# Performance work log

Measured on AMD Instinct MI355X. Metric: run time of the kernel, lower is better.

The kernel has to match this reference:

```python
import jax, jax.numpy as jnp
import numpy as np

B, L, D, H = 2, 2048, 1024, 16
DH = D // H  # 64


def setup_inputs() -> dict:
    key = jax.random.key(0)
    ks = jax.random.split(key, 11)
    s = 0.02
    return {
        "src": jax.random.normal(ks[0], (B, L, D), dtype=jnp.float32),
        "Wq": jax.random.normal(ks[1], (D, D), dtype=jnp.float32) * s,
        "bq": jax.random.normal(ks[2], (D,), dtype=jnp.float32) * s,
        "Wk": jax.random.normal(ks[3], (D, D), dtype=jnp.float32) * s,
        "bk": jax.random.normal(ks[4], (D,), dtype=jnp.float32) * s,
        "Wv": jax.random.normal(ks[5], (D, D), dtype=jnp.float32) * s,
        "bv": jax.random.normal(ks[6], (D,), dtype=jnp.float32) * s,
        "Wo": jax.random.normal(ks[7], (D, D), dtype=jnp.float32) * s,
        "bo": jax.random.normal(ks[8], (D,), dtype=jnp.float32) * s,
        "conv_w": jax.random.normal(ks[9], (H, D, 3), dtype=jnp.float32) * s,  # Conv1d weight [out=H, in=D, k=3]
        "conv_b": jax.random.normal(ks[10], (H,), dtype=jnp.float32) * s,
    }


def reference(src, Wq, bq, Wk, bk, Wv, bv, Wo, bo, conv_w, conv_b):
    b, l, d = src.shape
    h, dh = H, DH
    # QKV projections (torch Linear: x @ W.T + b), split into heads: [B,H,L,DH]
    Q = (src @ Wq.T + bq).reshape(b, l, h, dh).transpose(0, 2, 1, 3)
    K = (src @ Wk.T + bk).reshape(b, l, h, dh).transpose(0, 2, 1, 3)
    V = (src @ Wv.T + bv).reshape(b, l, h, dh).transpose(0, 2, 1, 3)
    # saliency conv: Conv1d(D->H, k=3, padding='same') on [B,D,L] -> [B,H,L]
    sal = jax.lax.conv_general_dilated(
        src.transpose(0, 2, 1), conv_w,
        window_strides=(1,), padding=[(1, 1)],
        dimension_numbers=("NCH", "OIH", "NCH"),
    ) + conv_b[None, :, None]
    # attention scores + per-head saliency bias (broadcast over query axis)
    scores = jnp.einsum("bhqd,bhkd->bhqk", Q, K) / jnp.sqrt(jnp.float32(dh))
    scores = scores + sal[:, :, None, :]
    attn = jax.nn.softmax(scores, axis=-1)  # dropout is identity in eval
    out = jnp.einsum("bhqk,bhkd->bhqd", attn, V)  # [B,H,L,DH]
    out = out.transpose(0, 2, 1, 3).reshape(b, l, d)
    out = out @ Wo.T + bo
    return out, attn
```

## Files before the change

kernel.cpp:

```cpp
#include <hip/hip_runtime.h>

typedef __bf16 bf16x8 __attribute__((ext_vector_type(8)));
typedef float f32x4 __attribute__((ext_vector_type(4)));
typedef unsigned short u16;
typedef unsigned int u32;

#define MFMA(a, b, c) __builtin_amdgcn_mfma_f32_16x16x32_bf16((a), (b), (c), 0, 0, 0)


__device__ __forceinline__ u16 f2bf(float f) {
  u32 u = __float_as_uint(f);
  return (u16)((u + 0x7fffu + ((u >> 16) & 1u)) >> 16);
}

__global__ __launch_bounds__(256) void prep_all(
    const float4* __restrict__ src, const float4* __restrict__ wq,
    const float4* __restrict__ wk, const float4* __restrict__ wv,
    const float4* __restrict__ wo, const float* __restrict__ cw,
    uint2* __restrict__ srcb, uint2* __restrict__ wqb, uint2* __restrict__ wkb,
    uint2* __restrict__ wvb, uint2* __restrict__ wob, float* __restrict__ cwT) {
  int bx = blockIdx.x;
  if (bx < 8192) {
    const float4* in;
    uint2* out;
    int base;
    if (bx < 4096) { in = src; out = srcb; base = 0; }
    else if (bx < 5120) { in = wq; out = wqb; base = 4096; }
    else if (bx < 6144) { in = wk; out = wkb; base = 5120; }
    else if (bx < 7168) { in = wv; out = wvb; base = 6144; }
    else { in = wo; out = wob; base = 7168; }
    int i = (bx - base) * 256 + threadIdx.x;
    float4 v = in[i];
    uint2 o;
    o.x = (u32)f2bf(v.x) | ((u32)f2bf(v.y) << 16);
    o.y = (u32)f2bf(v.z) | ((u32)f2bf(v.w) << 16);
    out[i] = o;
  } else {
    int i = (bx - 8192) * 256 + threadIdx.x;
    int h = i / 3072;
    int j = (i - h * 3072) >> 10;
    int d = i & 1023;
    cwT[i] = cw[(h * 1024 + d) * 3 + j];
  }
}

__global__ __launch_bounds__(256) void conv_sal_k(const float* __restrict__ src,
                                                  const float* __restrict__ cwT,
                                                  const float* __restrict__ cb,
                                                  float* __restrict__ sal) {
  const int t = threadIdx.x;
  const int h = t & 15, li = t >> 4;
  const int b = blockIdx.y;
  const int l = blockIdx.x * 16 + li;
  float4 acc = {0.f, 0.f, 0.f, 0.f};
#pragma unroll
  for (int j = 0; j < 3; j++) {
    int ls = l + j - 1;
    if (ls < 0 || ls >= 2048) continue;
    const float4* sp = (const float4*)(src + ((size_t)b * 2048 + ls) * 1024);
    const float4* wp = (const float4*)(cwT + (h * 3 + j) * 1024);
    for (int d = 0; d < 256; d++) {
      float4 a = sp[d], w = wp[d];
      acc.x += a.x * w.x;
      acc.y += a.y * w.y;
      acc.z += a.z * w.z;
      acc.w += a.w * w.w;
    }
  }
  sal[(b * 16 + h) * 2048 + l] = cb[h] + ((acc.x + acc.y) + (acc.z + acc.w));
}

__device__ __forceinline__ void gemm_core(const u16* __restrict__ Xg, const u16* __restrict__ Wg,
                                          int mblk, int nblk, u16* smA, u16* smB,
                                          f32x4 acc[4][4]) {
  const int t = threadIdx.x;
  const int lane = t & 63, wid = t >> 6;
  const int cl = lane & 15, gp = lane >> 4;
  const int r0 = t >> 2, cc = (t & 3) * 8;
  const u16* gA0 = Xg + (size_t)(mblk + r0) * 1024 + cc;
  const u16* gB0 = Wg + (size_t)(nblk + r0) * 1024 + cc;
  u16* lA0 = smA + t * 8;
  u16* lB0 = smB + t * 8;
  const u16* rA = smA + ((wid >> 1) * 64 + cl) * 32 + gp * 8;
  const u16* rB = smB + ((wid & 1) * 64 + cl) * 32 + gp * 8;
  for (int k0 = 0; k0 < 1024; k0 += 32) {
    bf16x8 sa0 = *(const bf16x8*)(gA0 + k0);
    bf16x8 sa1 = *(const bf16x8*)(gA0 + 64 * 1024 + k0);
    bf16x8 sb0 = *(const bf16x8*)(gB0 + k0);
    bf16x8 sb1 = *(const bf16x8*)(gB0 + 64 * 1024 + k0);
    __syncthreads();
    *(bf16x8*)lA0 = sa0;
    *(bf16x8*)(lA0 + 2048) = sa1;
    *(bf16x8*)lB0 = sb0;
    *(bf16x8*)(lB0 + 2048) = sb1;
    __syncthreads();
    bf16x8 a[4], b[4];
#pragma unroll
    for (int i = 0; i < 4; i++) {
      a[i] = *(const bf16x8*)(rA + i * 512);
      b[i] = *(const bf16x8*)(rB + i * 512);
    }
#pragma unroll
    for (int tm = 0; tm < 4; tm++)
#pragma unroll
      for (int tn = 0; tn < 4; tn++) acc[tm][tn] = MFMA(a[tm], b[tn], acc[tm][tn]);
  }
}

__global__ __launch_bounds__(256) void qkv_gemm(
    const u16* __restrict__ Xb, const u16* __restrict__ Wqb, const u16* __restrict__ Wkb,
    const u16* __restrict__ Wvb, const float* __restrict__ bq, const float* __restrict__ bk,
    const float* __restrict__ bv, u16* __restrict__ Qb, u16* __restrict__ Kb,
    u16* __restrict__ Vt) {
  __shared__ __align__(16) u16 smA[4096], smB[4096];
  const int seg = blockIdx.x >> 3;
  const u16* __restrict__ W = (seg == 0) ? Wqb : (seg == 1) ? Wkb : Wvb;
  const float* __restrict__ bias = (seg == 0) ? bq : (seg == 1) ? bk : bv;
  const int lane = threadIdx.x & 63, wid = threadIdx.x >> 6;
  const int cl = lane & 15, gp = lane >> 4;
  const int mblk = blockIdx.y * 128, nblk = (blockIdx.x & 7) * 128;
  const int m0 = mblk + (wid >> 1) * 64;
  const int n0 = nblk + (wid & 1) * 64;
  f32x4 acc[4][4] = {};
  gemm_core(Xb, W, mblk, nblk, smA, smB, acc);
#pragma unroll
  for (int tn = 0; tn < 4; tn++) {
    int col = n0 + tn * 16 + cl;
    float bv_ = bias[col];
    int hh = col >> 6, dh = col & 63;
#pragma unroll
    for (int tm = 0; tm < 4; tm++) {
#pragma unroll
      for (int r = 0; r < 4; r++) {
        int row = m0 + tm * 16 + gp * 4 + r;
        u16 hv = f2bf(acc[tm][tn][r] + bv_);
        int bb = row >> 11, l = row & 2047;
        if (seg == 0)
          Qb[(((size_t)(bb * 16 + hh) * 2048 + l) << 6) + dh] = hv;
        else if (seg == 1)
          Kb[(((size_t)(bb * 16 + hh) * 2048 + l) << 6) + dh] = hv;
        else
          Vt[((size_t)(bb * 16 + hh) * 64 + dh) * 2048 + l] = hv;
      }
    }
  }
}

__global__ __launch_bounds__(256) void out_gemm(const u16* __restrict__ Xb,
                                                const u16* __restrict__ W,
                                                const float* __restrict__ bias,
                                                float* __restrict__ Y) {
  __shared__ __align__(16) u16 smA[4096], smB[4096];
  const int lane = threadIdx.x & 63, wid = threadIdx.x >> 6;
  const int cl = lane & 15, gp = lane >> 4;
  const int mblk = blockIdx.y * 128, nblk = blockIdx.x * 128;
  const int m0 = mblk + (wid >> 1) * 64;
  const int n0 = nblk + (wid & 1) * 64;
  f32x4 acc[4][4] = {};
  gemm_core(Xb, W, mblk, nblk, smA, smB, acc);
#pragma unroll
  for (int tn = 0; tn < 4; tn++) {
    int col = n0 + tn * 16 + cl;
    float bv_ = bias[col];
#pragma unroll
    for (int tm = 0; tm < 4; tm++)
#pragma unroll
      for (int r = 0; r < 4; r++) {
        int row = m0 + tm * 16 + gp * 4 + r;
        Y[(size_t)row * 1024 + col] = acc[tm][tn][r] + bv_;
      }
  }
}

__global__ __launch_bounds__(256) void flash_fused(const u16* __restrict__ Qb,
                                                   const u16* __restrict__ Kb,
                                                   const u16* __restrict__ Vt,
                                                   const float* __restrict__ sal,
                                                   float* __restrict__ attn,
                                                   u16* __restrict__ Ob) {
  __shared__ __align__(16) u16 pbuf[4][16][72];
  const int bh = blockIdx.x;
  const int b = bh >> 4, h = bh & 15;
  const int lane = threadIdx.x & 63, wid = threadIdx.x >> 6;
  const int cl = lane & 15, gp = lane >> 4;
  const int q0 = blockIdx.y * 64 + wid * 16;
  const u16* Qh = Qb + (size_t)bh * 2048 * 64;
  const u16* Kh = Kb + (size_t)bh * 2048 * 64;
  const u16* Vh = Vt + (size_t)bh * 64 * 2048;
  const float* salh = sal + bh * 2048;
  bf16x8 aQ0 = *(const bf16x8*)(Qh + (size_t)(q0 + cl) * 64 + gp * 8);
  bf16x8 aQ1 = *(const bf16x8*)(Qh + (size_t)(q0 + cl) * 64 + 32 + gp * 8);
  float m[4], l[4];
#pragma unroll
  for (int r = 0; r < 4; r++) { m[r] = -1e30f; l[r] = 0.f; }

  for (int kb = 0; kb < 2048; kb += 64) {
    f32x4 st[4];
#pragma unroll
    for (int tn = 0; tn < 4; tn++) {
      const u16* kp = Kh + (size_t)(kb + tn * 16 + cl) * 64 + gp * 8;
      f32x4 s = {};
      s = MFMA(aQ0, *(const bf16x8*)kp, s);
      s = MFMA(aQ1, *(const bf16x8*)(kp + 32), s);
      st[tn] = s;
    }
#pragma unroll
    for (int tn = 0; tn < 4; tn++) {
      float sv = salh[kb + tn * 16 + cl];
#pragma unroll
      for (int r = 0; r < 4; r++) st[tn][r] = st[tn][r] * 0.125f + sv;
    }
#pragma unroll
    for (int r = 0; r < 4; r++) {
      float v = fmaxf(fmaxf(st[0][r], st[1][r]), fmaxf(st[2][r], st[3][r]));
      v = fmaxf(v, __shfl_xor(v, 1));
      v = fmaxf(v, __shfl_xor(v, 2));
      v = fmaxf(v, __shfl_xor(v, 4));
      v = fmaxf(v, __shfl_xor(v, 8));
      float mn = fmaxf(m[r], v);
      float alpha = __expf(m[r] - mn);
      m[r] = mn;
      float s0 = 0.f;
#pragma unroll
      for (int tn = 0; tn < 4; tn++) s0 += __expf(st[tn][r] - mn);
      s0 += __shfl_xor(s0, 1);
      s0 += __shfl_xor(s0, 2);
      s0 += __shfl_xor(s0, 4);
      s0 += __shfl_xor(s0, 8);
      l[r] = l[r] * alpha + s0;
    }
  }
  float il[4];
#pragma unroll
  for (int r = 0; r < 4; r++) il[r] = 1.0f / l[r];

  f32x4 oacc[4] = {};
  float* arow = attn + (size_t)bh * 2048 * 2048;
  u16* pw = &pbuf[wid][0][0];
  for (int kb = 0; kb < 2048; kb += 64) {
    f32x4 st[4];
#pragma unroll
    for (int tn = 0; tn < 4; tn++) {
      const u16* kp = Kh + (size_t)(kb + tn * 16 + cl) * 64 + gp * 8;
      f32x4 s = {};
      s = MFMA(aQ0, *(const bf16x8*)kp, s);
      s = MFMA(aQ1, *(const bf16x8*)(kp + 32), s);
      st[tn] = s;
    }
#pragma unroll
    for (int tn = 0; tn < 4; tn++) {
      float sv = salh[kb + tn * 16 + cl];
#pragma unroll
      for (int r = 0; r < 4; r++) {
        float p = __expf(st[tn][r] * 0.125f + sv - m[r]);
        arow[(size_t)(q0 + gp * 4 + r) * 2048 + kb + tn * 16 + cl] = p * il[r];
        pw[(gp * 4 + r) * 72 + tn * 16 + cl] = f2bf(p);
      }
    }
    __syncthreads();
    bf16x8 aP0 = *(const bf16x8*)(pw + cl * 72 + gp * 8);
    bf16x8 aP1 = *(const bf16x8*)(pw + cl * 72 + 32 + gp * 8);
#pragma unroll
    for (int tn = 0; tn < 4; tn++) {
      const u16* vp = Vh + (size_t)(tn * 16 + cl) * 2048 + kb + gp * 8;
      oacc[tn] = MFMA(aP0, *(const bf16x8*)vp, oacc[tn]);
      oacc[tn] = MFMA(aP1, *(const bf16x8*)(vp + 32), oacc[tn]);
    }
    __syncthreads();
  }
#pragma unroll
  for (int tn = 0; tn < 4; tn++) {
    int d = h * 64 + tn * 16 + cl;
#pragma unroll
    for (int r = 0; r < 4; r++) {
      int q = q0 + gp * 4 + r;
      Ob[((size_t)(b * 2048 + q)) * 1024 + d] = f2bf(oacc[tn][r] * il[r]);
    }
  }
}

extern "C" void kernel_launch(void* const* d_in, const int* in_sizes, int n_in,
                              void* d_out, int out_size, void* d_ws, size_t ws_size,
                              hipStream_t stream) {
  const float* src = (const float*)d_in[0];
  const float* Wq = (const float*)d_in[1];
  const float* bq = (const float*)d_in[2];
  const float* Wk = (const float*)d_in[3];
  const float* bk = (const float*)d_in[4];
  const float* Wv = (const float*)d_in[5];
  const float* bv = (const float*)d_in[6];
  const float* Wo = (const float*)d_in[7];
  const float* bo = (const float*)d_in[8];
  const float* cw = (const float*)d_in[9];
  const float* cb = (const float*)d_in[10];

  char* ws = (char*)d_ws;
  u16* srcb = (u16*)(ws + 0);
  u16* wqb = (u16*)(ws + 8388608);
  u16* wkb = (u16*)(ws + 10485760);
  u16* wvb = (u16*)(ws + 12582912);
  u16* wob = (u16*)(ws + 14680064);
  u16* Qb = (u16*)(ws + 16777216);
  u16* Kb = (u16*)(ws + 25165824);
  u16* Vt = (u16*)(ws + 33554432);
  u16* Ob = (u16*)(ws + 41943040);
  float* cwT = (float*)(ws + 50331648);
  float* sal = (float*)(ws + 50528256);

  float* outp = (float*)d_out;
  float* attn = (float*)d_out + 4194304;

  prep_all<<<8384, 256, 0, stream>>>((const float4*)src, (const float4*)Wq, (const float4*)Wk,
                                     (const float4*)Wv, (const float4*)Wo, cw,
                                     (uint2*)srcb, (uint2*)wqb, (uint2*)wkb, (uint2*)wvb,
                                     (uint2*)wob, cwT);
  conv_sal_k<<<dim3(128, 2), 256, 0, stream>>>(src, cwT, cb, sal);
  qkv_gemm<<<dim3(24, 32), 256, 0, stream>>>(srcb, wqb, wkb, wvb, bq, bk, bv, Qb, Kb, Vt);
  flash_fused<<<dim3(32, 32), 256, 0, stream>>>(Qb, Kb, Vt, sal, attn, Ob);
  out_gemm<<<dim3(8, 32), 256, 0, stream>>>(Ob, wob, bo, outp);
}
```

Measured before the change: 1.078 ms.

## Split conv reduction across waves, shrink flash blocks, defer row reductions, drop barriers

The saliency conv now splits the D reduction across four waves and combines partial sums through shared memory, which launches four times as many blocks for more parallelism. The flash attention kernel moves to 128-thread blocks over twice as many query tiles, with a launch-bounds occupancy hint. Its first pass keeps per-lane running max and sum and merges them across lanes only once at the end, instead of shuffling every iteration. The block-wide barriers around the P staging buffer are replaced by a wave-local LDS wait, which relies on each wave touching only its own slice of the buffer.

After: 1.100 ms. Within noise of the previous version (+2.0%).

```diff
diff --git a/kernel.cpp b/kernel.cpp
--- a/kernel.cpp
+++ b/kernel.cpp
@@ -48,18 +48,21 @@
                                                   const float* __restrict__ cwT,
                                                   const float* __restrict__ cb,
                                                   float* __restrict__ sal) {
+  __shared__ float part[4][16][17];
   const int t = threadIdx.x;
-  const int h = t & 15, li = t >> 4;
+  const int h = t & 15;
+  const int li = (t >> 4) & 3;
+  const int dc = t >> 6;
   const int b = blockIdx.y;
-  const int l = blockIdx.x * 16 + li;
+  const int l = blockIdx.x * 4 + li;
   float4 acc = {0.f, 0.f, 0.f, 0.f};
 #pragma unroll
   for (int j = 0; j < 3; j++) {
     int ls = l + j - 1;
     if (ls < 0 || ls >= 2048) continue;
-    const float4* sp = (const float4*)(src + ((size_t)b * 2048 + ls) * 1024);
-    const float4* wp = (const float4*)(cwT + (h * 3 + j) * 1024);
-    for (int d = 0; d < 256; d++) {
+    const float4* sp = (const float4*)(src + ((size_t)b * 2048 + ls) * 1024 + dc * 256);
+    const float4* wp = (const float4*)(cwT + (h * 3 + j) * 1024 + dc * 256);
+    for (int d = 0; d < 64; d++) {
       float4 a = sp[d], w = wp[d];
       acc.x += a.x * w.x;
       acc.y += a.y * w.y;
@@ -67,7 +70,12 @@
       acc.w += a.w * w.w;
     }
   }
-  sal[(b * 16 + h) * 2048 + l] = cb[h] + ((acc.x + acc.y) + (acc.z + acc.w));
+  part[dc][li][h] = (acc.x + acc.y) + (acc.z + acc.w);
+  __syncthreads();
+  if (dc == 0) {
+    float s = cb[h] + ((part[0][li][h] + part[1][li][h]) + (part[2][li][h] + part[3][li][h]));
+    sal[(b * 16 + h) * 2048 + l] = s;
+  }
 }
 
 __device__ __forceinline__ void gemm_core(const u16* __restrict__ Xg, const u16* __restrict__ Wg,
@@ -172,28 +180,28 @@
   }
 }
 
-__global__ __launch_bounds__(256) void flash_fused(const u16* __restrict__ Qb,
-                                                   const u16* __restrict__ Kb,
-                                                   const u16* __restrict__ Vt,
-                                                   const float* __restrict__ sal,
-                                                   float* __restrict__ attn,
-                                                   u16* __restrict__ Ob) {
-  __shared__ __align__(16) u16 pbuf[4][16][72];
+__global__ __launch_bounds__(128, 6) void flash_fused(const u16* __restrict__ Qb,
+                                                      const u16* __restrict__ Kb,
+                                                      const u16* __restrict__ Vt,
+                                                      const float* __restrict__ sal,
+                                                      float* __restrict__ attn,
+                                                      u16* __restrict__ Ob) {
+  __shared__ __align__(16) u16 pbuf[2][16][72];
   const int bh = blockIdx.x;
   const int b = bh >> 4, h = bh & 15;
   const int lane = threadIdx.x & 63, wid = threadIdx.x >> 6;
   const int cl = lane & 15, gp = lane >> 4;
-  const int q0 = blockIdx.y * 64 + wid * 16;
+  const int q0 = blockIdx.y * 32 + wid * 16;
   const u16* Qh = Qb + (size_t)bh * 2048 * 64;
   const u16* Kh = Kb + (size_t)bh * 2048 * 64;
   const u16* Vh = Vt + (size_t)bh * 64 * 2048;
   const float* salh = sal + bh * 2048;
   bf16x8 aQ0 = *(const bf16x8*)(Qh + (size_t)(q0 + cl) * 64 + gp * 8);
   bf16x8 aQ1 = *(const bf16x8*)(Qh + (size_t)(q0 + cl) * 64 + 32 + gp * 8);
-  float m[4], l[4];
-#pragma unroll
-  for (int r = 0; r < 4; r++) { m[r] = -1e30f; l[r] = 0.f; }
-
+
+  float ml[4], ll[4];
+#pragma unroll
+  for (int r = 0; r < 4; r++) { ml[r] = -1e30f; ll[r] = 0.f; }
   for (int kb = 0; kb < 2048; kb += 64) {
     f32x4 st[4];
 #pragma unroll
@@ -213,26 +221,30 @@
 #pragma unroll
     for (int r = 0; r < 4; r++) {
       float v = fmaxf(fmaxf(st[0][r], st[1][r]), fmaxf(st[2][r], st[3][r]));
-      v = fmaxf(v, __shfl_xor(v, 1));
-      v = fmaxf(v, __shfl_xor(v, 2));
-      v = fmaxf(v, __shfl_xor(v, 4));
-      v = fmaxf(v, __shfl_xor(v, 8));
-      float mn = fmaxf(m[r], v);
-      float alpha = __expf(m[r] - mn);
-      m[r] = mn;
-      float s0 = 0.f;
-#pragma unroll
-      for (int tn = 0; tn < 4; tn++) s0 += __expf(st[tn][r] - mn);
-      s0 += __shfl_xor(s0, 1);
-      s0 += __shfl_xor(s0, 2);
-      s0 += __shfl_xor(s0, 4);
-      s0 += __shfl_xor(s0, 8);
-      l[r] = l[r] * alpha + s0;
-    }
-  }
-  float il[4];
-#pragma unroll
-  for (int r = 0; r < 4; r++) il[r] = 1.0f / l[r];
+      float mn = fmaxf(ml[r], v);
+      float alpha = __expf(ml[r] - mn);
+      ml[r] = mn;
+      float s0 = __expf(st[0][r] - mn) + __expf(st[1][r] - mn) + __expf(st[2][r] - mn) +
+                 __expf(st[3][r] - mn);
+      ll[r] = ll[r] * alpha + s0;
+    }
+  }
+  float m[4], il[4];
+#pragma unroll
+  for (int r = 0; r < 4; r++) {
+    float mr = ml[r];
+    mr = fmaxf(mr, __shfl_xor(mr, 1));
+    mr = fmaxf(mr, __shfl_xor(mr, 2));
+    mr = fmaxf(mr, __shfl_xor(mr, 4));
+    mr = fmaxf(mr, __shfl_xor(mr, 8));
+    float lr = ll[r] * __expf(ml[r] - mr);
+    lr += __shfl_xor(lr, 1);
+    lr += __shfl_xor(lr, 2);
+    lr += __shfl_xor(lr, 4);
+    lr += __shfl_xor(lr, 8);
+    m[r] = mr;
+    il[r] = 1.0f / lr;
+  }
 
   f32x4 oacc[4] = {};
   float* arow = attn + (size_t)bh * 2048 * 2048;
@@ -257,16 +269,17 @@
         pw[(gp * 4 + r) * 72 + tn * 16 + cl] = f2bf(p);
       }
     }
-    __syncthreads();
+    asm volatile("s_waitcnt lgkmcnt(0)" ::: "memory");
+    __builtin_amdgcn_sched_barrier(0);
     bf16x8 aP0 = *(const bf16x8*)(pw + cl * 72 + gp * 8);
     bf16x8 aP1 = *(const bf16x8*)(pw + cl * 72 + 32 + gp * 8);
+    asm volatile("" ::: "memory");
 #pragma unroll
     for (int tn = 0; tn < 4; tn++) {
       const u16* vp = Vh + (size_t)(tn * 16 + cl) * 2048 + kb + gp * 8;
       oacc[tn] = MFMA(aP0, *(const bf16x8*)vp, oacc[tn]);
       oacc[tn] = MFMA(aP1, *(const bf16x8*)(vp + 32), oacc[tn]);
     }
-    __syncthreads();
   }
 #pragma unroll
   for (int tn = 0; tn < 4; tn++) {
@@ -314,8 +327,8 @@
                                      (const float4*)Wv, (const float4*)Wo, cw,
                                      (uint2*)srcb, (uint2*)wqb, (uint2*)wkb, (uint2*)wvb,
                                      (uint2*)wob, cwT);
-  conv_sal_k<<<dim3(128, 2), 256, 0, stream>>>(src, cwT, cb, sal);
+  conv_sal_k<<<dim3(512, 2), 256, 0, stream>>>(src, cwT, cb, sal);
   qkv_gemm<<<dim3(24, 32), 256, 0, stream>>>(srcb, wqb, wkb, wvb, bq, bk, bv, Qb, Kb, Vt);
-  flash_fused<<<dim3(32, 32), 256, 0, stream>>>(Qb, Kb, Vt, sal, attn, Ob);
+  flash_fused<<<dim3(32, 64), 128, 0, stream>>>(Qb, Kb, Vt, sal, attn, Ob);
   out_gemm<<<dim3(8, 32), 256, 0, stream>>>(Ob, wob, bo, outp);
 }
```
